# Kernel optimization log

Hardware: AMD Instinct MI355X
Metric: run time of the kernel (lower is better)

The kernel has to match this reference:

```python
import jax, jax.numpy as jnp
import numpy as np

SR = 44100
K = 1.0 / SR                      # time step
LX = 0.5
MAX_OM = 10000.0 * 2.0 * np.pi    # fmax * 2pi
MIN_OM = 20.0 * 2.0 * np.pi
TAU0, TAU1 = 6.0, 1.0
OM2SQ = (2.0 * np.pi * 500.0) ** 2          # OmDamp2^2 (OmDamp1 = 0)
ALPHA = 3.0 * np.log(10.0) / OM2SQ * (OM2SQ / TAU0)   # = 3 ln10 / tau0
BETA = 3.0 * np.log(10.0) / OM2SQ * (1.0 / TAU1 - 1.0 / TAU0)
MU_SCALE, DMU_SCALE, T0MU_SCALE = 2.43, 0.002452, 0.004115
M_MAX = 80  # 80x80 = 6400 modes


def setup_inputs() -> dict:
    z = jnp.zeros((), dtype=jnp.float32)
    return {
        "mu_raw": z, "D_over_mu_raw": z, "T0_over_mu_raw": z,
        "Ly_raw": z, "xo_raw": z, "yo_raw": z,
        "num_samples": 22050,
    }


def _modal_ir(mu_raw, D_over_mu_raw, T0_over_mu_raw, Ly_raw, xo_raw, yo_raw, num_samples):
    sp, sg = jax.nn.softplus, jax.nn.sigmoid
    # physical parameters via differentiable bounds
    mu = (sp(mu_raw) + 1e-4) * MU_SCALE
    D_over_mu = (sp(D_over_mu_raw) + 1e-4) * DMU_SCALE
    T0_over_mu = (sp(T0_over_mu_raw) + 1e-4) * T0MU_SCALE
    Ly = 1.1 + (4.0 - 1.1) * sg(Ly_raw)
    xo = 0.49 * LX + (1.0 - 0.49) * LX * sg(xo_raw)
    yo = 0.51 * Ly + (1.0 - 0.51) * Ly * sg(yo_raw)
    xi = 0.1 * LX
    yi = 0.1 * Ly
    # mode grid [6400]
    idx = jnp.arange(1, M_MAX + 1, dtype=jnp.float32)
    gm, gn = jnp.meshgrid(idx, idx, indexing="ij")
    m, n = gm.ravel(), gn.ravel()
    g1 = (m * np.pi / LX) ** 2 + (n * np.pi / Ly) ** 2
    omega_sq = T0_over_mu * g1 + D_over_mu * g1 * g1
    omega = jnp.sqrt(jax.nn.relu(omega_sq))
    valid = ((omega <= MAX_OM) & (omega >= MIN_OM)).astype(omega.dtype)
    InW = jnp.cos(xi * np.pi * m / LX) * jnp.cos(yi * np.pi * n / Ly)
    OutW = jnp.cos(xo * np.pi * m / LX) * jnp.cos(yo * np.pi * n / Ly)
    sigma = ALPHA + BETA * omega ** 2
    ms = 0.25 * mu * LX * Ly
    P = OutW * InW * (K * K) * jnp.exp(-sigma * K) / ms * valid  # [modes]
    # time axis [T]
    t = jnp.arange(num_samples, dtype=jnp.float32)
    decay_env = jnp.exp(-sigma[:, None] * (t[None, :] - 1.0) * K)    # [modes, T]
    sine_num = jnp.sin(t[None, :] * omega[:, None] * K)              # [modes, T]
    sine_den = jnp.sin(omega * K) + 1e-8                             # [modes]
    mode_waveforms = P[:, None] * decay_env * (sine_num / sine_den[:, None])
    disp = jnp.sum(mode_waveforms, axis=0)                           # [T]
    peak = jnp.max(jnp.abs(disp)) + 1e-8
    return disp / peak


def reference(mu_raw, D_over_mu_raw, T0_over_mu_raw, Ly_raw, xo_raw, yo_raw, num_samples):
    return _modal_ir(mu_raw, D_over_mu_raw, T0_over_mu_raw, Ly_raw, xo_raw, yo_raw, num_samples)
```

## Files before the change

### kernel.cpp

```cpp
#include <hip/hip_runtime.h>
#include <math.h>

#define NMODES 6400
#define TB     256
#define MPT    25
#define TC     44

static __device__ __forceinline__ float softplusf(float x) {
    return log1pf(expf(-fabsf(x))) + fmaxf(x, 0.0f);
}
static __device__ __forceinline__ float sigmoidf(float x) {
    return 1.0f / (1.0f + expf(-x));
}

__global__ void setup_kernel(const float* __restrict__ mu_raw,
                             const float* __restrict__ Dmu_raw,
                             const float* __restrict__ T0mu_raw,
                             const float* __restrict__ Ly_raw,
                             const float* __restrict__ xo_raw,
                             const float* __restrict__ yo_raw,
                             float* __restrict__ wsA,
                             float* __restrict__ wsW,
                             float* __restrict__ wsS,
                             float* __restrict__ wsCW,
                             float* __restrict__ wsSW)
{
    int id = blockIdx.x * blockDim.x + threadIdx.x;
    if (id >= NMODES) return;

    const float KF   = 1.0f / 44100.0f;
    const float PI_F = (float)M_PI;
    const double om2sq = (2.0 * M_PI * 500.0) * (2.0 * M_PI * 500.0);
    const float ALPHA_F = (float)(3.0 * M_LN10 / om2sq * (om2sq / 6.0));
    const float BETA_F  = (float)(3.0 * M_LN10 / om2sq * (1.0 - 1.0 / 6.0));
    const float MAX_OM_F = (float)(10000.0 * 2.0 * M_PI);
    const float MIN_OM_F = (float)(20.0 * 2.0 * M_PI);
    const float KK_F = (float)((1.0 / 44100.0) * (1.0 / 44100.0));

    float mu   = (softplusf(mu_raw[0])   + 1e-4f) * 2.43f;
    float Dmu  = (softplusf(Dmu_raw[0])  + 1e-4f) * 0.002452f;
    float T0mu = (softplusf(T0mu_raw[0]) + 1e-4f) * 0.004115f;
    float Ly   = 1.1f + 2.9f * sigmoidf(Ly_raw[0]);
    float xo   = 0.245f + 0.255f * sigmoidf(xo_raw[0]);
    float yo   = __fadd_rn(__fmul_rn(0.51f, Ly),
                           __fmul_rn(__fmul_rn(0.49f, Ly), sigmoidf(yo_raw[0])));

    float mf = (float)(id / 80 + 1);
    float nf = (float)(id % 80 + 1);

    float am = __fmul_rn(__fmul_rn(mf, PI_F), 2.0f);
    float bn = __fdiv_rn(__fmul_rn(nf, PI_F), Ly);
    float g1 = __fadd_rn(__fmul_rn(am, am), __fmul_rn(bn, bn));
    float omega_sq = __fadd_rn(__fmul_rn(T0mu, g1),
                               __fmul_rn(__fmul_rn(Dmu, g1), g1));
    float omega = sqrtf(fmaxf(omega_sq, 0.0f));
    float valid = (omega <= MAX_OM_F && omega >= MIN_OM_F) ? 1.0f : 0.0f;

    float xi_pi = (float)(0.05 * M_PI);
    float yi = __fmul_rn(0.1f, Ly);
    float InW = __fmul_rn(
        cosf(__fmul_rn(__fmul_rn(xi_pi, mf), 2.0f)),
        cosf(__fdiv_rn(__fmul_rn(__fmul_rn(yi, PI_F), nf), Ly)));
    float OutW = __fmul_rn(
        cosf(__fmul_rn(__fmul_rn(__fmul_rn(xo, PI_F), mf), 2.0f)),
        cosf(__fdiv_rn(__fmul_rn(__fmul_rn(yo, PI_F), nf), Ly)));

    float sigma = __fadd_rn(ALPHA_F, __fmul_rn(BETA_F, __fmul_rn(omega, omega)));
    float ms = __fmul_rn(__fmul_rn(__fmul_rn(0.25f, mu), 0.5f), Ly);
    float P = __fmul_rn(
        __fdiv_rn(__fmul_rn(__fmul_rn(__fmul_rn(OutW, InW), KK_F),
                            expf(__fmul_rn(-sigma, KF))),
                  ms),
        valid);
    float den = __fadd_rn(sinf(__fmul_rn(omega, KF)), 1e-8f);
    float A = __fdiv_rn(P, den);

    const double Kd = 1.0 / 44100.0;
    double th = (double)omega * Kd;
    double dd = exp(-(double)sigma * Kd);
    wsA[id]  = A;
    wsW[id]  = omega;
    wsS[id]  = sigma;
    wsCW[id] = (float)(dd * cos(th));
    wsSW[id] = (float)(dd * sin(th));
}

__global__ __launch_bounds__(TB, 2) void accum_kernel(const float* __restrict__ wsA,
                                                      const float* __restrict__ wsW,
                                                      const float* __restrict__ wsS,
                                                      const float* __restrict__ wsCW,
                                                      const float* __restrict__ wsSW,
                                                      float* __restrict__ out, int T)
{
    const int tid = threadIdx.x;
    const int t0  = blockIdx.x * TC;

    const float  KF     = 1.0f / 44100.0f;
    const double Kd     = 1.0 / 44100.0;
    const double TWO_PI = 6.283185307179586476925286766559;
    const double I2PI   = 0.15915494309189533576888376337251;

    __shared__ float sRed[4][TC];

    float S[MPT], C[MPT], CW[MPT], SW[MPT];
    #pragma unroll
    for (int j = 0; j < MPT; ++j) {
        int m = j * TB + tid;
        float A  = wsA[m];
        float w  = wsW[m];
        float sg = wsS[m];
        CW[j] = wsCW[m];
        SW[j] = wsSW[m];
        double ph = (double)t0 * (double)w * Kd;
        double q  = rint(ph * I2PI);
        float  r  = (float)fma(-q, TWO_PI, ph);
        float env = A * __expf(-sg * (float)(t0 - 1) * KF);
        S[j] = env * __sinf(r);
        C[j] = env * __cosf(r);
    }

    const int wv = tid >> 6, lane = tid & 63;

    #pragma unroll 1
    for (int tt = 0; tt < TC; ++tt) {
        float a0 = S[0], a1 = S[1], a2 = S[2], a3 = S[3];
        #pragma unroll
        for (int j = 4; j < MPT; j += 4) a0 += S[j];
        #pragma unroll
        for (int j = 5; j < MPT; j += 4) a1 += S[j];
        #pragma unroll
        for (int j = 6; j < MPT; j += 4) a2 += S[j];
        #pragma unroll
        for (int j = 7; j < MPT; j += 4) a3 += S[j];
        float acc = (a0 + a1) + (a2 + a3);
        #pragma unroll
        for (int j = 0; j < MPT; ++j) {
            float nS = __fmaf_rn(S[j], CW[j],  C[j] * SW[j]);
            float nC = __fmaf_rn(C[j], CW[j], -(S[j] * SW[j]));
            S[j] = nS;
            C[j] = nC;
        }
        #pragma unroll
        for (int off = 32; off > 0; off >>= 1)
            acc += __shfl_xor(acc, off, 64);
        if (lane == 0) sRed[wv][tt] = acc;
    }
    __syncthreads();
    for (int tt = tid; tt < TC; tt += TB) {
        int t = t0 + tt;
        if (t < T)
            out[t] = (sRed[0][tt] + sRed[1][tt]) + (sRed[2][tt] + sRed[3][tt]);
    }
}

__global__ __launch_bounds__(1024) void norm_kernel(float* __restrict__ out, int T)
{
    __shared__ float red[16];
    __shared__ float peakv;
    float mx = 0.0f;
    for (int i = threadIdx.x; i < T; i += 1024) mx = fmaxf(mx, fabsf(out[i]));
    #pragma unroll
    for (int off = 32; off > 0; off >>= 1)
        mx = fmaxf(mx, __shfl_xor(mx, off, 64));
    int lane = threadIdx.x & 63, wv = threadIdx.x >> 6;
    if (lane == 0) red[wv] = mx;
    __syncthreads();
    if (threadIdx.x == 0) {
        float m = red[0];
        #pragma unroll
        for (int i = 1; i < 16; ++i) m = fmaxf(m, red[i]);
        peakv = m + 1e-8f;
    }
    __syncthreads();
    float pk = peakv;
    for (int i = threadIdx.x; i < T; i += 1024) out[i] = __fdiv_rn(out[i], pk);
}

extern "C" void kernel_launch(void* const* d_in, const int* in_sizes, int n_in,
                              void* d_out, int out_size, void* d_ws, size_t ws_size,
                              hipStream_t stream)
{
    const float* mu   = (const float*)d_in[0];
    const float* Dmu  = (const float*)d_in[1];
    const float* T0mu = (const float*)d_in[2];
    const float* Lyr  = (const float*)d_in[3];
    const float* xor_ = (const float*)d_in[4];
    const float* yor_ = (const float*)d_in[5];
    float* out = (float*)d_out;

    float* ws   = (float*)d_ws;
    float* wsA  = ws;
    float* wsW  = ws + NMODES;
    float* wsS  = ws + 2 * NMODES;
    float* wsCW = ws + 3 * NMODES;
    float* wsSW = ws + 4 * NMODES;

    int T = out_size;
    int tchunks = (T + TC - 1) / TC;

    setup_kernel<<<(NMODES + TB - 1) / TB, TB, 0, stream>>>(mu, Dmu, T0mu, Lyr, xor_, yor_,
                                                            wsA, wsW, wsS, wsCW, wsSW);
    accum_kernel<<<tchunks, TB, 0, stream>>>(wsA, wsW, wsS, wsCW, wsSW, out, T);
    norm_kernel<<<1, 1024, 0, stream>>>(out, T);
}
```

Measured before the change: 103.0 us.

## Fuse setup, accumulation and normalization into a single kernel with last-block reduction

Merges the three kernels into one. Each block recomputes the per-mode parameters (omega, sigma, weights, rotation factors) in registers instead of reading them from workspace. The final peak normalization is done by the last block to finish, detected through an atomic counter that is reset by a memset before launch. This removes two kernel launches and the workspace round trip, but every block (about 500 of them) now repeats the transcendental setup work for all 6400 modes. Finishing the normalization in a single 256-thread block is also serialized, and the rotation factors are now computed in single precision.

```diff
diff --git a/kernel.cpp b/kernel.cpp
--- a/kernel.cpp
+++ b/kernel.cpp
@@ -13,29 +13,31 @@
     return 1.0f / (1.0f + expf(-x));
 }
 
-__global__ void setup_kernel(const float* __restrict__ mu_raw,
-                             const float* __restrict__ Dmu_raw,
-                             const float* __restrict__ T0mu_raw,
-                             const float* __restrict__ Ly_raw,
-                             const float* __restrict__ xo_raw,
-                             const float* __restrict__ yo_raw,
-                             float* __restrict__ wsA,
-                             float* __restrict__ wsW,
-                             float* __restrict__ wsS,
-                             float* __restrict__ wsCW,
-                             float* __restrict__ wsSW)
+__global__ __launch_bounds__(TB, 2) void plate_kernel(
+    const float* __restrict__ mu_raw,
+    const float* __restrict__ Dmu_raw,
+    const float* __restrict__ T0mu_raw,
+    const float* __restrict__ Ly_raw,
+    const float* __restrict__ xo_raw,
+    const float* __restrict__ yo_raw,
+    float* __restrict__ out,
+    unsigned int* __restrict__ cnt,
+    int T)
 {
-    int id = blockIdx.x * blockDim.x + threadIdx.x;
-    if (id >= NMODES) return;
+    const int tid = threadIdx.x;
+    const int t0  = blockIdx.x * TC;
 
     const float KF   = 1.0f / 44100.0f;
     const float PI_F = (float)M_PI;
     const double om2sq = (2.0 * M_PI * 500.0) * (2.0 * M_PI * 500.0);
-    const float ALPHA_F = (float)(3.0 * M_LN10 / om2sq * (om2sq / 6.0));
-    const float BETA_F  = (float)(3.0 * M_LN10 / om2sq * (1.0 - 1.0 / 6.0));
+    const float ALPHA_F  = (float)(3.0 * M_LN10 / om2sq * (om2sq / 6.0));
+    const float BETA_F   = (float)(3.0 * M_LN10 / om2sq * (1.0 - 1.0 / 6.0));
     const float MAX_OM_F = (float)(10000.0 * 2.0 * M_PI);
     const float MIN_OM_F = (float)(20.0 * 2.0 * M_PI);
-    const float KK_F = (float)((1.0 / 44100.0) * (1.0 / 44100.0));
+    const float KK_F     = (float)((1.0 / 44100.0) * (1.0 / 44100.0));
+    const double Kd      = 1.0 / 44100.0;
+    const double TWO_PI  = 6.283185307179586476925286766559;
+    const double I2PI    = 0.15915494309189533576888376337251;
 
     float mu   = (softplusf(mu_raw[0])   + 1e-4f) * 2.43f;
     float Dmu  = (softplusf(Dmu_raw[0])  + 1e-4f) * 0.002452f;
@@ -44,79 +46,59 @@
     float xo   = 0.245f + 0.255f * sigmoidf(xo_raw[0]);
     float yo   = __fadd_rn(__fmul_rn(0.51f, Ly),
                            __fmul_rn(__fmul_rn(0.49f, Ly), sigmoidf(yo_raw[0])));
-
-    float mf = (float)(id / 80 + 1);
-    float nf = (float)(id % 80 + 1);
-
-    float am = __fmul_rn(__fmul_rn(mf, PI_F), 2.0f);
-    float bn = __fdiv_rn(__fmul_rn(nf, PI_F), Ly);
-    float g1 = __fadd_rn(__fmul_rn(am, am), __fmul_rn(bn, bn));
-    float omega_sq = __fadd_rn(__fmul_rn(T0mu, g1),
-                               __fmul_rn(__fmul_rn(Dmu, g1), g1));
-    float omega = sqrtf(fmaxf(omega_sq, 0.0f));
-    float valid = (omega <= MAX_OM_F && omega >= MIN_OM_F) ? 1.0f : 0.0f;
-
     float xi_pi = (float)(0.05 * M_PI);
-    float yi = __fmul_rn(0.1f, Ly);
-    float InW = __fmul_rn(
-        cosf(__fmul_rn(__fmul_rn(xi_pi, mf), 2.0f)),
-        cosf(__fdiv_rn(__fmul_rn(__fmul_rn(yi, PI_F), nf), Ly)));
-    float OutW = __fmul_rn(
-        cosf(__fmul_rn(__fmul_rn(__fmul_rn(xo, PI_F), mf), 2.0f)),
-        cosf(__fdiv_rn(__fmul_rn(__fmul_rn(yo, PI_F), nf), Ly)));
-
-    float sigma = __fadd_rn(ALPHA_F, __fmul_rn(BETA_F, __fmul_rn(omega, omega)));
-    float ms = __fmul_rn(__fmul_rn(__fmul_rn(0.25f, mu), 0.5f), Ly);
-    float P = __fmul_rn(
-        __fdiv_rn(__fmul_rn(__fmul_rn(__fmul_rn(OutW, InW), KK_F),
-                            expf(__fmul_rn(-sigma, KF))),
-                  ms),
-        valid);
-    float den = __fadd_rn(sinf(__fmul_rn(omega, KF)), 1e-8f);
-    float A = __fdiv_rn(P, den);
-
-    const double Kd = 1.0 / 44100.0;
-    double th = (double)omega * Kd;
-    double dd = exp(-(double)sigma * Kd);
-    wsA[id]  = A;
-    wsW[id]  = omega;
-    wsS[id]  = sigma;
-    wsCW[id] = (float)(dd * cos(th));
-    wsSW[id] = (float)(dd * sin(th));
-}
-
-__global__ __launch_bounds__(TB, 2) void accum_kernel(const float* __restrict__ wsA,
-                                                      const float* __restrict__ wsW,
-                                                      const float* __restrict__ wsS,
-                                                      const float* __restrict__ wsCW,
-                                                      const float* __restrict__ wsSW,
-                                                      float* __restrict__ out, int T)
-{
-    const int tid = threadIdx.x;
-    const int t0  = blockIdx.x * TC;
-
-    const float  KF     = 1.0f / 44100.0f;
-    const double Kd     = 1.0 / 44100.0;
-    const double TWO_PI = 6.283185307179586476925286766559;
-    const double I2PI   = 0.15915494309189533576888376337251;
+    float yi    = __fmul_rn(0.1f, Ly);
+    float ms    = __fmul_rn(__fmul_rn(__fmul_rn(0.25f, mu), 0.5f), Ly);
 
     __shared__ float sRed[4][TC];
+    __shared__ float red[4];
+    __shared__ int   sLast;
 
     float S[MPT], C[MPT], CW[MPT], SW[MPT];
     #pragma unroll
     for (int j = 0; j < MPT; ++j) {
         int m = j * TB + tid;
-        float A  = wsA[m];
-        float w  = wsW[m];
-        float sg = wsS[m];
-        CW[j] = wsCW[m];
-        SW[j] = wsSW[m];
+        float mf = (float)(m / 80 + 1);
+        float nf = (float)(m % 80 + 1);
+
+        float am = __fmul_rn(__fmul_rn(mf, PI_F), 2.0f);
+        float bn = __fdiv_rn(__fmul_rn(nf, PI_F), Ly);
+        float g1 = __fadd_rn(__fmul_rn(am, am), __fmul_rn(bn, bn));
+        float omega_sq = __fadd_rn(__fmul_rn(T0mu, g1),
+                                   __fmul_rn(__fmul_rn(Dmu, g1), g1));
+        float w = sqrtf(fmaxf(omega_sq, 0.0f));
+        float valid = (w <= MAX_OM_F && w >= MIN_OM_F) ? 1.0f : 0.0f;
+
+        float InW = __fmul_rn(
+            cosf(__fmul_rn(__fmul_rn(xi_pi, mf), 2.0f)),
+            cosf(__fdiv_rn(__fmul_rn(__fmul_rn(yi, PI_F), nf), Ly)));
+        float OutW = __fmul_rn(
+            cosf(__fmul_rn(__fmul_rn(__fmul_rn(xo, PI_F), mf), 2.0f)),
+            cosf(__fdiv_rn(__fmul_rn(__fmul_rn(yo, PI_F), nf), Ly)));
+
+        float sigma = __fadd_rn(ALPHA_F, __fmul_rn(BETA_F, __fmul_rn(w, w)));
+        float P = __fmul_rn(
+            __fdiv_rn(__fmul_rn(__fmul_rn(__fmul_rn(OutW, InW), KK_F),
+                                expf(__fmul_rn(-sigma, KF))),
+                      ms),
+            valid);
+        float den = __fadd_rn(sinf(__fmul_rn(w, KF)), 1e-8f);
+        float A = __fdiv_rn(P, den);
+
+        float ds  = __expf(__fmul_rn(-sigma, KF));
+        float sth, cth;
+        sincosf(__fmul_rn(w, KF), &sth, &cth);
+        CW[j] = __fmul_rn(ds, cth);
+        SW[j] = __fmul_rn(ds, sth);
+
         double ph = (double)t0 * (double)w * Kd;
         double q  = rint(ph * I2PI);
         float  r  = (float)fma(-q, TWO_PI, ph);
-        float env = A * __expf(-sg * (float)(t0 - 1) * KF);
-        S[j] = env * __sinf(r);
-        C[j] = env * __cosf(r);
+        float s0, c0;
+        __sincosf(r, &s0, &c0);
+        float env = A * __expf(-sigma * (float)(t0 - 1) * KF);
+        S[j] = env * s0;
+        C[j] = env * c0;
     }
 
     const int wv = tid >> 6, lane = tid & 63;
@@ -151,29 +133,26 @@
         if (t < T)
             out[t] = (sRed[0][tt] + sRed[1][tt]) + (sRed[2][tt] + sRed[3][tt]);
     }
-}
 
-__global__ __launch_bounds__(1024) void norm_kernel(float* __restrict__ out, int T)
-{
-    __shared__ float red[16];
-    __shared__ float peakv;
-    float mx = 0.0f;
-    for (int i = threadIdx.x; i < T; i += 1024) mx = fmaxf(mx, fabsf(out[i]));
-    #pragma unroll
-    for (int off = 32; off > 0; off >>= 1)
-        mx = fmaxf(mx, __shfl_xor(mx, off, 64));
-    int lane = threadIdx.x & 63, wv = threadIdx.x >> 6;
-    if (lane == 0) red[wv] = mx;
+    __threadfence();
     __syncthreads();
-    if (threadIdx.x == 0) {
-        float m = red[0];
-        #pragma unroll
-        for (int i = 1; i < 16; ++i) m = fmaxf(m, red[i]);
-        peakv = m + 1e-8f;
+    if (tid == 0) {
+        unsigned int old = atomicAdd(cnt, 1u);
+        sLast = (old == gridDim.x - 1) ? 1 : 0;
     }
     __syncthreads();
-    float pk = peakv;
-    for (int i = threadIdx.x; i < T; i += 1024) out[i] = __fdiv_rn(out[i], pk);
+    if (sLast) {
+        __threadfence();
+        float mx = 0.0f;
+        for (int i = tid; i < T; i += TB) mx = fmaxf(mx, fabsf(out[i]));
+        #pragma unroll
+        for (int off = 32; off > 0; off >>= 1)
+            mx = fmaxf(mx, __shfl_xor(mx, off, 64));
+        if (lane == 0) red[wv] = mx;
+        __syncthreads();
+        float pk = fmaxf(fmaxf(red[0], red[1]), fmaxf(red[2], red[3])) + 1e-8f;
+        for (int i = tid; i < T; i += TB) out[i] = __fdiv_rn(out[i], pk);
+    }
 }
 
 extern "C" void kernel_launch(void* const* d_in, const int* in_sizes, int n_in,
@@ -187,19 +166,11 @@
     const float* xor_ = (const float*)d_in[4];
     const float* yor_ = (const float*)d_in[5];
     float* out = (float*)d_out;
-
-    float* ws   = (float*)d_ws;
-    float* wsA  = ws;
-    float* wsW  = ws + NMODES;
-    float* wsS  = ws + 2 * NMODES;
-    float* wsCW = ws + 3 * NMODES;
-    float* wsSW = ws + 4 * NMODES;
+    unsigned int* cnt = (unsigned int*)d_ws;
 
     int T = out_size;
     int tchunks = (T + TC - 1) / TC;
 
-    setup_kernel<<<(NMODES + TB - 1) / TB, TB, 0, stream>>>(mu, Dmu, T0mu, Lyr, xor_, yor_,
-                                                            wsA, wsW, wsS, wsCW, wsSW);
-    accum_kernel<<<tchunks, TB, 0, stream>>>(wsA, wsW, wsS, wsCW, wsSW, out, T);
-    norm_kernel<<<1, 1024, 0, stream>>>(out, T);
+    hipMemsetAsync(cnt, 0, sizeof(unsigned int), stream);
+    plate_kernel<<<tchunks, TB, 0, stream>>>(mu, Dmu, T0mu, Lyr, xor_, yor_, out, cnt, T);
 }
```

After: 160.6 us. 56.0% more time.

## Split modes across a second grid dimension and combine partial sums with atomics

Applied to the files above, without the earlier changes.

The accumulation kernel now splits the 6400 modes into 5 groups along blockIdx.y, each thread holding 5 modes instead of 25, with larger time chunks. Per-wave partial sums are written straight to the output with atomicAdd after a memset, replacing the shared-memory cross-wave reduction and __syncthreads. Several timesteps are batched so their shuffle reductions interleave. This cuts register pressure and raises the number of blocks for better occupancy, at the cost of many more atomics, an extra memset, and run-to-run variation in float summation order.

```diff
diff --git a/kernel.cpp b/kernel.cpp
--- a/kernel.cpp
+++ b/kernel.cpp
@@ -3,8 +3,10 @@
 
 #define NMODES 6400
 #define TB     256
-#define MPT    25
-#define TC     44
+#define MPT    5
+#define MG     5
+#define BATCH  4
+#define TC     84
 
 static __device__ __forceinline__ float softplusf(float x) {
     return log1pf(expf(-fabsf(x))) + fmaxf(x, 0.0f);
@@ -31,11 +33,11 @@
     const float KF   = 1.0f / 44100.0f;
     const float PI_F = (float)M_PI;
     const double om2sq = (2.0 * M_PI * 500.0) * (2.0 * M_PI * 500.0);
-    const float ALPHA_F = (float)(3.0 * M_LN10 / om2sq * (om2sq / 6.0));
-    const float BETA_F  = (float)(3.0 * M_LN10 / om2sq * (1.0 - 1.0 / 6.0));
+    const float ALPHA_F  = (float)(3.0 * M_LN10 / om2sq * (om2sq / 6.0));
+    const float BETA_F   = (float)(3.0 * M_LN10 / om2sq * (1.0 - 1.0 / 6.0));
     const float MAX_OM_F = (float)(10000.0 * 2.0 * M_PI);
     const float MIN_OM_F = (float)(20.0 * 2.0 * M_PI);
-    const float KK_F = (float)((1.0 / 44100.0) * (1.0 / 44100.0));
+    const float KK_F     = (float)((1.0 / 44100.0) * (1.0 / 44100.0));
 
     float mu   = (softplusf(mu_raw[0])   + 1e-4f) * 2.43f;
     float Dmu  = (softplusf(Dmu_raw[0])  + 1e-4f) * 0.002452f;
@@ -85,27 +87,27 @@
     wsSW[id] = (float)(dd * sin(th));
 }
 
-__global__ __launch_bounds__(TB, 2) void accum_kernel(const float* __restrict__ wsA,
-                                                      const float* __restrict__ wsW,
-                                                      const float* __restrict__ wsS,
-                                                      const float* __restrict__ wsCW,
-                                                      const float* __restrict__ wsSW,
-                                                      float* __restrict__ out, int T)
-{
-    const int tid = threadIdx.x;
-    const int t0  = blockIdx.x * TC;
+__global__ __launch_bounds__(TB) void accum_kernel(
+    const float* __restrict__ wsA,
+    const float* __restrict__ wsW,
+    const float* __restrict__ wsS,
+    const float* __restrict__ wsCW,
+    const float* __restrict__ wsSW,
+    float* __restrict__ out, int T)
+{
+    const int tid  = threadIdx.x;
+    const int t0   = blockIdx.x * TC;
+    const int base = blockIdx.y * (TB * MPT);
 
     const float  KF     = 1.0f / 44100.0f;
     const double Kd     = 1.0 / 44100.0;
     const double TWO_PI = 6.283185307179586476925286766559;
     const double I2PI   = 0.15915494309189533576888376337251;
 
-    __shared__ float sRed[4][TC];
-
     float S[MPT], C[MPT], CW[MPT], SW[MPT];
     #pragma unroll
     for (int j = 0; j < MPT; ++j) {
-        int m = j * TB + tid;
+        int m = base + j * TB + tid;
         float A  = wsA[m];
         float w  = wsW[m];
         float sg = wsS[m];
@@ -114,42 +116,43 @@
         double ph = (double)t0 * (double)w * Kd;
         double q  = rint(ph * I2PI);
         float  r  = (float)fma(-q, TWO_PI, ph);
+        float s0, c0;
+        __sincosf(r, &s0, &c0);
         float env = A * __expf(-sg * (float)(t0 - 1) * KF);
-        S[j] = env * __sinf(r);
-        C[j] = env * __cosf(r);
+        S[j] = env * s0;
+        C[j] = env * c0;
     }
 
-    const int wv = tid >> 6, lane = tid & 63;
+    const int lane = tid & 63;
 
     #pragma unroll 1
-    for (int tt = 0; tt < TC; ++tt) {
-        float a0 = S[0], a1 = S[1], a2 = S[2], a3 = S[3];
+    for (int it = 0; it < TC; it += BATCH) {
+        float acc[BATCH];
         #pragma unroll
-        for (int j = 4; j < MPT; j += 4) a0 += S[j];
-        #pragma unroll
-        for (int j = 5; j < MPT; j += 4) a1 += S[j];
-        #pragma unroll
-        for (int j = 6; j < MPT; j += 4) a2 += S[j];
-        #pragma unroll
-        for (int j = 7; j < MPT; j += 4) a3 += S[j];
-        float acc = (a0 + a1) + (a2 + a3);
-        #pragma unroll
-        for (int j = 0; j < MPT; ++j) {
-            float nS = __fmaf_rn(S[j], CW[j],  C[j] * SW[j]);
-            float nC = __fmaf_rn(C[j], CW[j], -(S[j] * SW[j]));
-            S[j] = nS;
-            C[j] = nC;
+        for (int b = 0; b < BATCH; ++b) {
+            float a01 = S[0] + S[1];
+            float a23 = S[2] + S[3];
+            acc[b] = (a01 + a23) + S[4];
+            #pragma unroll
+            for (int j = 0; j < MPT; ++j) {
+                float nS = __fmaf_rn(S[j], CW[j],  C[j] * SW[j]);
+                float nC = __fmaf_rn(C[j], CW[j], -(S[j] * SW[j]));
+                S[j] = nS;
+                C[j] = nC;
+            }
         }
         #pragma unroll
-        for (int off = 32; off > 0; off >>= 1)
-            acc += __shfl_xor(acc, off, 64);
-        if (lane == 0) sRed[wv][tt] = acc;
-    }
-    __syncthreads();
-    for (int tt = tid; tt < TC; tt += TB) {
-        int t = t0 + tt;
-        if (t < T)
-            out[t] = (sRed[0][tt] + sRed[1][tt]) + (sRed[2][tt] + sRed[3][tt]);
+        for (int off = 32; off > 0; off >>= 1) {
+            #pragma unroll
+            for (int b = 0; b < BATCH; ++b)
+                acc[b] += __shfl_xor(acc[b], off, 64);
+        }
+        if (lane == 0) {
+            int t = t0 + it;
+            #pragma unroll
+            for (int b = 0; b < BATCH; ++b)
+                if (t + b < T) atomicAdd(&out[t + b], acc[b]);
+        }
     }
 }
 
@@ -198,8 +201,9 @@
     int T = out_size;
     int tchunks = (T + TC - 1) / TC;
 
+    hipMemsetAsync(out, 0, (size_t)T * sizeof(float), stream);
     setup_kernel<<<(NMODES + TB - 1) / TB, TB, 0, stream>>>(mu, Dmu, T0mu, Lyr, xor_, yor_,
                                                             wsA, wsW, wsS, wsCW, wsSW);
-    accum_kernel<<<tchunks, TB, 0, stream>>>(wsA, wsW, wsS, wsCW, wsSW, out, T);
+    accum_kernel<<<dim3(tchunks, MG), TB, 0, stream>>>(wsA, wsW, wsS, wsCW, wsSW, out, T);
     norm_kernel<<<1, 1024, 0, stream>>>(out, T);
 }
```

Result: slower. 122.6 us (+19.1%).
